# Kernel tuning notes

Measured on AMD Instinct MI355X. Metric: run time of the kernel, lower is better.

## Reference

```python
import jax, jax.numpy as jnp
import numpy as np

N = 50000   # nodes
E = 200000  # edges (avg degree ~4, pose-graph-like sparsity)
F_IN = 512
NEG_SLOPE = 0.01  # F.leaky_relu default


def _softmax_aggr(src_feat, dst, num_nodes):
    # torch_geometric SoftmaxAggregation(t=1): per-destination, per-feature
    # alpha = softmax(x_j), out = sum_j alpha * x_j
    m = jax.ops.segment_max(src_feat, dst, num_segments=num_nodes)  # [N,F]
    m = jnp.where(jnp.isfinite(m), m, 0.0)  # empty segments -> -inf guard
    e = jnp.exp(src_feat - m[dst])                                   # [E,F]
    denom = jax.ops.segment_sum(e, dst, num_segments=num_nodes)      # [N,F]
    num = jax.ops.segment_sum(e * src_feat, dst, num_segments=num_nodes)
    return num / jnp.maximum(denom, 1e-16)  # 0 for isolated nodes


def setup_inputs() -> dict:
    key = jax.random.key(0)
    ks = jax.random.split(key, 9)
    inp = {
        "x": jax.random.normal(ks[0], (N, F_IN), dtype=jnp.float32),
        "W1_rel": jax.random.normal(ks[1], (513, 256), dtype=jnp.float32) * 0.04,
        "b1_rel": jnp.zeros((256,), dtype=jnp.float32),
        "W1_root": jax.random.normal(ks[2], (513, 256), dtype=jnp.float32) * 0.04,
        "W2_rel": jax.random.normal(ks[3], (257, 64), dtype=jnp.float32) * 0.06,
        "b2_rel": jnp.zeros((64,), dtype=jnp.float32),
        "W2_root": jax.random.normal(ks[4], (257, 64), dtype=jnp.float32) * 0.06,
        "Wp": jax.random.normal(ks[5], (65, 3), dtype=jnp.float32) * 0.1,
        "bp": jnp.zeros((3,), dtype=jnp.float32),
        "Wr": jax.random.normal(ks[6], (65, 4), dtype=jnp.float32) * 0.1,
        "br": jnp.zeros((4,), dtype=jnp.float32),
        "edge_index": jax.random.randint(ks[7], (2, E), 0, N, dtype=jnp.int64),
    }
    return inp


def reference(x, W1_rel, b1_rel, W1_root, W2_rel, b2_rel, W2_root,
              Wp, bp, Wr, br, edge_index):
    src, dst = edge_index[0], edge_index[1]
    node_index = jnp.arange(x.shape[0], dtype=x.dtype)[:, None]  # [N,1]

    # dropout is identity in eval mode
    h = jnp.concatenate([x, node_index], axis=1)  # [N,513]

    # GraphConv(513,256, aggr='softmax'): lin_rel(softmax_aggr(x_j)) + lin_root(x)
    agg1 = _softmax_aggr(h[src], dst, x.shape[0])               # [N,513]
    h = agg1 @ W1_rel + b1_rel + h @ W1_root                     # [N,256]
    h = jnp.where(h >= 0, h, NEG_SLOPE * h)

    h = jnp.concatenate([h, node_index], axis=1)  # [N,257]

    # GraphConv(257,64) default aggr='add'
    agg2 = jax.ops.segment_sum(h[src], dst, num_segments=x.shape[0])  # [N,257]
    h = agg2 @ W2_rel + b2_rel + h @ W2_root                           # [N,64]
    h = jnp.where(h >= 0, h, NEG_SLOPE * h)

    h = jnp.concatenate([h, node_index], axis=1)  # [N,65]

    position = h @ Wp + bp                         # [N,3]
    rotation = h @ Wr + br                         # [N,4]
    norm = jnp.linalg.norm(rotation, axis=1, keepdims=True)
    rotation = rotation / jnp.maximum(norm, 1e-12)  # F.normalize

    return jnp.concatenate([position, rotation], axis=1)  # [N,7]
```

## Files before the change

kernel.cpp:

```cpp
#include <hip/hip_runtime.h>

#define NNODES 50000
#define NEDGES 200000
#define NSCANB ((NNODES + 255) / 256)

typedef short  bf16x8 __attribute__((ext_vector_type(8)));
typedef float  f32x4  __attribute__((ext_vector_type(4)));
typedef unsigned int u32x4 __attribute__((ext_vector_type(4)));

__device__ __forceinline__ unsigned short f2bf(float f) {
    union { float f; unsigned int u; } c; c.f = f;
    unsigned int r = c.u + 0x7fffu + ((c.u >> 16) & 1u);
    return (unsigned short)(r >> 16);
}
__device__ __forceinline__ float bflo(unsigned int v) {
    union { unsigned int u; float f; } c; c.u = v << 16;
    return c.f;
}
__device__ __forceinline__ float bfhi(unsigned int v) {
    union { unsigned int u; float f; } c; c.u = v & 0xffff0000u;
    return c.f;
}

#define PREP_B1 (256 * 1024)
#define PREP_B2 (64 * 512)
#define PREP_XC (NNODES * 64)
__global__ __launch_bounds__(256) void k_prepcount(const float* __restrict__ x,
                                                   const float* __restrict__ W1_rel,
                                                   const float* __restrict__ W1_root,
                                                   const float* __restrict__ W2_rel,
                                                   const float* __restrict__ W2_root,
                                                   const int* __restrict__ ei,
                                                   int* __restrict__ deg,
                                                   unsigned short* __restrict__ Bt1,
                                                   unsigned short* __restrict__ Bt2,
                                                   unsigned short* __restrict__ xb) {
    const int gtid = blockIdx.x * 256 + threadIdx.x;
    const int GS = gridDim.x * 256;
    for (int e = gtid; e < NEDGES; e += GS) atomicAdd(&deg[ei[NEDGES + e]], 1);
    for (int i = gtid; i < PREP_B1; i += GS) {
        int n = i >> 10, k = i & 1023;
        float v = (k < 512) ? W1_rel[k * 256 + n] : W1_root[(k - 512) * 256 + n];
        Bt1[i] = f2bf(v);
    }
    for (int i = gtid; i < PREP_B2; i += GS) {
        int n = i >> 9, k = i & 511;
        float v = (k < 256) ? W2_rel[k * 64 + n] : W2_root[(k - 256) * 64 + n];
        Bt2[i] = f2bf(v);
    }
    for (int i = gtid; i < PREP_XC; i += GS) {
        int n = i >> 6, c8 = (i & 63) * 8;
        const float* xp = x + (size_t)n * 512 + c8;
        float4 a = *(const float4*)xp;
        float4 bb = *(const float4*)(xp + 4);
        unsigned short o[8];
        o[0] = f2bf(a.x); o[1] = f2bf(a.y); o[2] = f2bf(a.z); o[3] = f2bf(a.w);
        o[4] = f2bf(bb.x); o[5] = f2bf(bb.y); o[6] = f2bf(bb.z); o[7] = f2bf(bb.w);
        *(u32x4*)(xb + (size_t)n * 512 + c8) = *(const u32x4*)o;
    }
}

__global__ __launch_bounds__(256) void k_scanA(const int* __restrict__ deg,
                                               int* __restrict__ rs,
                                               int* __restrict__ partials) {
    __shared__ int sm[256];
    int t = threadIdx.x, i = blockIdx.x * 256 + t;
    int v = (i < NNODES) ? deg[i] : 0;
    sm[t] = v;
    __syncthreads();
#pragma unroll
    for (int off = 1; off < 256; off <<= 1) {
        int u = (t >= off) ? sm[t - off] : 0;
        __syncthreads();
        sm[t] += u;
        __syncthreads();
    }
    if (i < NNODES) rs[i] = sm[t] - v;
    if (t == 255) partials[blockIdx.x] = sm[255];
}

__global__ __launch_bounds__(256) void k_scanC2(int* __restrict__ rs,
                                                const int* __restrict__ partials,
                                                int* __restrict__ cursor) {
    __shared__ int sm[256];
    int t = threadIdx.x, b = blockIdx.x;
    sm[t] = (t < b && t < NSCANB) ? partials[t] : 0;
    __syncthreads();
#pragma unroll
    for (int off = 128; off; off >>= 1) {
        if (t < off) sm[t] += sm[t + off];
        __syncthreads();
    }
    int off0 = sm[0];
    int i = b * 256 + t;
    if (i < NNODES) {
        int rv = rs[i] + off0;
        rs[i] = rv;
        cursor[i] = rv;
    }
    if (i == 0) rs[NNODES] = NEDGES;
}

__global__ void k_scatter(const int* __restrict__ ei, int* __restrict__ cursor,
                          int* __restrict__ srcs) {
    int e = blockIdx.x * 256 + threadIdx.x;
    if (e < NEDGES) {
        int d = ei[NEDGES + e];
        int p = atomicAdd(&cursor[d], 1);
        srcs[p] = ei[e];
    }
}

__global__ __launch_bounds__(256) void k_agg1(const unsigned short* __restrict__ xb,
                                              const int* __restrict__ rs,
                                              const int* __restrict__ srcs,
                                              unsigned short* __restrict__ AggBuf) {
    int wv = threadIdx.x >> 6;
    int lane = threadIdx.x & 63;
    int n = blockIdx.x * 4 + wv;
    int e0 = rs[n], e1 = rs[n + 1];
    float nu[8], de[8];
#pragma unroll
    for (int j = 0; j < 8; ++j) { nu[j] = 0.f; de[j] = 0.f; }

    auto accum = [&](u32x4 r) {
#pragma unroll
        for (int p = 0; p < 4; ++p) {
            float v0 = bflo(r[p]), v1 = bfhi(r[p]);
            float E0 = __expf(v0), E1 = __expf(v1);
            de[2 * p] += E0; nu[2 * p] += E0 * v0;
            de[2 * p + 1] += E1; nu[2 * p + 1] += E1 * v1;
        }
    };

    int e = e0;
    for (; e + 3 < e1; e += 4) {
        int s0 = srcs[e], s1 = srcs[e + 1], s2 = srcs[e + 2], s3 = srcs[e + 3];
        u32x4 r0 = *(const u32x4*)(xb + (size_t)s0 * 512 + lane * 8);
        u32x4 r1 = *(const u32x4*)(xb + (size_t)s1 * 512 + lane * 8);
        u32x4 r2 = *(const u32x4*)(xb + (size_t)s2 * 512 + lane * 8);
        u32x4 r3 = *(const u32x4*)(xb + (size_t)s3 * 512 + lane * 8);
        accum(r0); accum(r1); accum(r2); accum(r3);
    }
    if (e + 1 < e1) {
        int s0 = srcs[e], s1 = srcs[e + 1];
        u32x4 r0 = *(const u32x4*)(xb + (size_t)s0 * 512 + lane * 8);
        u32x4 r1 = *(const u32x4*)(xb + (size_t)s1 * 512 + lane * 8);
        accum(r0); accum(r1);
        e += 2;
    }
    if (e < e1) {
        u32x4 r0 = *(const u32x4*)(xb + (size_t)srcs[e] * 512 + lane * 8);
        accum(r0);
    }
    unsigned short o[8];
#pragma unroll
    for (int j = 0; j < 8; ++j) o[j] = f2bf(nu[j] / fmaxf(de[j], 1e-16f));
    *(u32x4*)(AggBuf + (size_t)n * 512 + lane * 8) = *(const u32x4*)o;
}

__global__ __launch_bounds__(256) void k_agg2(const int* __restrict__ rs,
                                              const int* __restrict__ srcs,
                                              const unsigned short* __restrict__ H1,
                                              unsigned short* __restrict__ Seg) {
    int wv = threadIdx.x >> 6;
    int lane = threadIdx.x & 63;
    int n = blockIdx.x * 4 + wv;
    int e0 = rs[n], e1 = rs[n + 1];
    float a[4] = {0.f, 0.f, 0.f, 0.f};

    auto accum = [&](uint2 r) {
        a[0] += bflo(r.x); a[1] += bfhi(r.x);
        a[2] += bflo(r.y); a[3] += bfhi(r.y);
    };

    int e = e0;
    for (; e + 3 < e1; e += 4) {
        int s0 = srcs[e], s1 = srcs[e + 1], s2 = srcs[e + 2], s3 = srcs[e + 3];
        uint2 r0 = *(const uint2*)(H1 + (size_t)s0 * 256 + lane * 4);
        uint2 r1 = *(const uint2*)(H1 + (size_t)s1 * 256 + lane * 4);
        uint2 r2 = *(const uint2*)(H1 + (size_t)s2 * 256 + lane * 4);
        uint2 r3 = *(const uint2*)(H1 + (size_t)s3 * 256 + lane * 4);
        accum(r0); accum(r1); accum(r2); accum(r3);
    }
    if (e + 1 < e1) {
        int s0 = srcs[e], s1 = srcs[e + 1];
        uint2 r0 = *(const uint2*)(H1 + (size_t)s0 * 256 + lane * 4);
        uint2 r1 = *(const uint2*)(H1 + (size_t)s1 * 256 + lane * 4);
        accum(r0); accum(r1);
        e += 2;
    }
    if (e < e1) {
        uint2 r0 = *(const uint2*)(H1 + (size_t)srcs[e] * 256 + lane * 4);
        accum(r0);
    }
    uint2 o;
    o.x = (unsigned int)f2bf(a[0]) | ((unsigned int)f2bf(a[1]) << 16);
    o.y = (unsigned int)f2bf(a[2]) | ((unsigned int)f2bf(a[3]) << 16);
    *(uint2*)(Seg + (size_t)n * 256 + lane * 4) = o;
}

__global__ __launch_bounds__(256) void k_gemm1(const unsigned short* __restrict__ A1,
                                               const unsigned short* __restrict__ A2,
                                               const unsigned short* __restrict__ Bt,
                                               const int* __restrict__ rs,
                                               const int* __restrict__ srcs,
                                               const float* __restrict__ r1,
                                               const float* __restrict__ r2,
                                               const float* __restrict__ bias,
                                               unsigned short* __restrict__ outp) {
    constexpr int BM = 64, BN = 128, BK = 64;
    __shared__ __align__(16) unsigned short As[2][BM * BK];
    __shared__ __align__(16) unsigned short Bs[2][BN * BK];
    __shared__ float s1t[BM];

    const int tid = threadIdx.x;
    const int w = tid >> 6;
    const int lane = tid & 63;
    const int lm = lane & 15;
    const int quad = lane >> 4;
    const int wr = w >> 1;
    const int wc = w & 1;
    const int rowbase = blockIdx.y * BM;
    const int colbase = blockIdx.x * BN;
    const int wrow = wr * 32;
    const int wcol = wc * 64;

    const int rsub = lane >> 3;
    const int csw = (lane & 7) ^ rsub;

    f32x4 acc[2][4];
#pragma unroll
    for (int mi = 0; mi < 2; ++mi)
#pragma unroll
        for (int ni = 0; ni < 4; ++ni) acc[mi][ni] = (f32x4){0.f, 0.f, 0.f, 0.f};

    auto stage = [&](unsigned short* Asb, unsigned short* Bsb, int kt) {
        const unsigned short* Ab = (kt < 512) ? A1 : A2;
        int kof = (kt < 512) ? kt : kt - 512;
#pragma unroll
        for (int l = 0; l < 2; ++l) {
            int r = w * 16 + l * 8;
            int gr = rowbase + r + rsub;
            if (gr >= NNODES) gr = NNODES - 1;
            const unsigned short* gp = Ab + (size_t)gr * 512 + kof + csw * 8;
            __builtin_amdgcn_global_load_lds(
                (const __attribute__((address_space(1))) void*)gp,
                (__attribute__((address_space(3))) void*)(Asb + r * BK), 16, 0, 0);
        }
#pragma unroll
        for (int l = 0; l < 4; ++l) {
            int r = w * 32 + l * 8;
            const unsigned short* gp = Bt + (size_t)(colbase + r + rsub) * 1024 + kt + csw * 8;
            __builtin_amdgcn_global_load_lds(
                (const __attribute__((address_space(1))) void*)gp,
                (__attribute__((address_space(3))) void*)(Bsb + r * BK), 16, 0, 0);
        }
    };

    auto compute = [&](const unsigned short* Asb, const unsigned short* Bsb) {
#pragma unroll
        for (int kk = 0; kk < BK; kk += 32) {
            const int kidx = (kk >> 3) + quad;
            const int phys = kidx ^ (lm & 7);
            bf16x8 af[2], bfr[4];
#pragma unroll
            for (int mi = 0; mi < 2; ++mi)
                af[mi] = __builtin_bit_cast(bf16x8,
                    *(const u32x4*)(Asb + (wrow + mi * 16 + lm) * BK + phys * 8));
#pragma unroll
            for (int ni = 0; ni < 4; ++ni)
                bfr[ni] = __builtin_bit_cast(bf16x8,
                    *(const u32x4*)(Bsb + (wcol + ni * 16 + lm) * BK + phys * 8));
#pragma unroll
            for (int mi = 0; mi < 2; ++mi)
#pragma unroll
                for (int ni = 0; ni < 4; ++ni)
                    acc[mi][ni] = __builtin_amdgcn_mfma_f32_16x16x32_bf16(
                        af[mi], bfr[ni], acc[mi][ni], 0, 0, 0);
        }
    };

    stage(As[0], Bs[0], 0);
#pragma unroll 1
    for (int t = 0; t < 16; t += 2) {
        stage(As[1], Bs[1], (t + 1) * BK);
        asm volatile("s_waitcnt vmcnt(6)" ::: "memory");
        __builtin_amdgcn_s_barrier();
        __builtin_amdgcn_sched_barrier(0);
        compute(As[0], Bs[0]);
        __builtin_amdgcn_s_barrier();
        if (t + 2 < 16) {
            stage(As[0], Bs[0], (t + 2) * BK);
            asm volatile("s_waitcnt vmcnt(6)" ::: "memory");
        } else {
            asm volatile("s_waitcnt vmcnt(0)" ::: "memory");
        }
        __builtin_amdgcn_s_barrier();
        __builtin_amdgcn_sched_barrier(0);
        compute(As[1], Bs[1]);
        __builtin_amdgcn_s_barrier();
    }

    if (tid < BM) {
        int grow = rowbase + tid;
        float r_ = 0.f;
        if (grow < NNODES) {
            int e0 = rs[grow], e1 = rs[grow + 1];
            float m = -INFINITY, d = 0.f, q = 0.f;
            for (int e = e0; e < e1; ++e) {
                float v = (float)srcs[e];
                float nm = fmaxf(m, v);
                float sc = __expf(m - nm), ee = __expf(v - nm);
                d = d * sc + ee;
                q = q * sc + ee * v;
                m = nm;
            }
            r_ = q / fmaxf(d, 1e-16f);
        }
        s1t[tid] = r_;
    }
    __syncthreads();

#pragma unroll
    for (int ni = 0; ni < 4; ++ni) {
        int gc = colbase + wcol + ni * 16 + lm;
        float r1v = r1[gc], r2v = r2[gc], bv = bias[gc];
#pragma unroll
        for (int mi = 0; mi < 2; ++mi) {
#pragma unroll
            for (int r = 0; r < 4; ++r) {
                int lrow = wrow + mi * 16 + quad * 4 + r;
                int grow = rowbase + lrow;
                if (grow < NNODES) {
                    float v = acc[mi][ni][r] + s1t[lrow] * r1v + (float)grow * r2v + bv;
                    v = (v >= 0.f) ? v : 0.01f * v;
                    outp[(size_t)grow * 256 + gc] = f2bf(v);
                }
            }
        }
    }
}

__global__ __launch_bounds__(256) void k_gemm2h(const unsigned short* __restrict__ A1,
                                                const unsigned short* __restrict__ A2,
                                                const unsigned short* __restrict__ Bt,
                                                const int* __restrict__ rs,
                                                const int* __restrict__ srcs,
                                                const float* __restrict__ r1,
                                                const float* __restrict__ r2,
                                                const float* __restrict__ bias,
                                                const float* __restrict__ Wp,
                                                const float* __restrict__ bp,
                                                const float* __restrict__ Wr,
                                                const float* __restrict__ br,
                                                float* __restrict__ out) {
    constexpr int BM = 64, BN = 64, BK = 64;
    __shared__ __align__(16) unsigned short As[BM * BK];
    __shared__ __align__(16) unsigned short Bs[BN * BK];
    __shared__ float h2t[BM * 65];
    __shared__ float s1t[BM];

    const int tid = threadIdx.x;
    const int w = tid >> 6;
    const int lane = tid & 63;
    const int lm = lane & 15;
    const int quad = lane >> 4;
    const int rowbase = blockIdx.x * BM;
    const int wrow = w * 16;

    const int rsub = lane >> 3;
    const int csw = (lane & 7) ^ rsub;

    f32x4 acc[4];
#pragma unroll
    for (int ni = 0; ni < 4; ++ni) acc[ni] = (f32x4){0.f, 0.f, 0.f, 0.f};

    for (int kt = 0; kt < 512; kt += BK) {
        const unsigned short* Ab = (kt < 256) ? A1 : A2;
        int kof = (kt < 256) ? kt : kt - 256;
#pragma unroll
        for (int l = 0; l < 2; ++l) {
            int r = w * 16 + l * 8;
            int gr = rowbase + r + rsub;
            if (gr >= NNODES) gr = NNODES - 1;
            const unsigned short* gp = Ab + (size_t)gr * 256 + kof + csw * 8;
            __builtin_amdgcn_global_load_lds(
                (const __attribute__((address_space(1))) void*)gp,
                (__attribute__((address_space(3))) void*)(As + r * BK), 16, 0, 0);
        }
#pragma unroll
        for (int l = 0; l < 2; ++l) {
            int r = w * 16 + l * 8;
            const unsigned short* gp = Bt + (size_t)(r + rsub) * 512 + kt + csw * 8;
            __builtin_amdgcn_global_load_lds(
                (const __attribute__((address_space(1))) void*)gp,
                (__attribute__((address_space(3))) void*)(Bs + r * BK), 16, 0, 0);
        }
        __syncthreads();
#pragma unroll
        for (int kk = 0; kk < BK; kk += 32) {
            const int kidx = (kk >> 3) + quad;
            const int phys = kidx ^ (lm & 7);
            bf16x8 af;
            af = __builtin_bit_cast(bf16x8,
                *(const u32x4*)(As + (wrow + lm) * BK + phys * 8));
            bf16x8 bfr[4];
#pragma unroll
            for (int ni = 0; ni < 4; ++ni)
                bfr[ni] = __builtin_bit_cast(bf16x8,
                    *(const u32x4*)(Bs + (ni * 16 + lm) * BK + phys * 8));
#pragma unroll
            for (int ni = 0; ni < 4; ++ni)
                acc[ni] = __builtin_amdgcn_mfma_f32_16x16x32_bf16(
                    af, bfr[ni], acc[ni], 0, 0, 0);
        }
        __syncthreads();
    }

    if (tid < BM) {
        int grow = rowbase + tid;
        float si = 0.f;
        if (grow < NNODES) {
            int e0 = rs[grow], e1 = rs[grow + 1];
            for (int e = e0; e < e1; ++e) si += (float)srcs[e];
        }
        s1t[tid] = si;
    }
    __syncthreads();

#pragma unroll
    for (int ni = 0; ni < 4; ++ni) {
        int gc = ni * 16 + lm;
        float r1v = r1[gc], r2v = r2[gc], bv = bias[gc];
#pragma unroll
        for (int r = 0; r < 4; ++r) {
            int lrow = wrow + quad * 4 + r;
            int grow = rowbase + lrow;
            float v = acc[ni][r] + s1t[lrow] * r1v + (float)grow * r2v + bv;
            v = (v >= 0.f) ? v : 0.01f * v;
            h2t[lrow * 65 + gc] = v;
        }
    }
    __syncthreads();

    if (tid < BM) {
        int grow = rowbase + tid;
        if (grow < NNODES) {
            const float* hv = h2t + tid * 65;
            float idx = (float)grow;
            float p0 = 0.f, p1 = 0.f, p2 = 0.f;
            float r0 = 0.f, r1a = 0.f, r2a = 0.f, r3 = 0.f;
#pragma unroll 8
            for (int c = 0; c < 64; ++c) {
                float v = hv[c];
                p0 += v * Wp[c * 3 + 0];
                p1 += v * Wp[c * 3 + 1];
                p2 += v * Wp[c * 3 + 2];
                r0 += v * Wr[c * 4 + 0];
                r1a += v * Wr[c * 4 + 1];
                r2a += v * Wr[c * 4 + 2];
                r3 += v * Wr[c * 4 + 3];
            }
            p0 += idx * Wp[64 * 3 + 0] + bp[0];
            p1 += idx * Wp[64 * 3 + 1] + bp[1];
            p2 += idx * Wp[64 * 3 + 2] + bp[2];
            r0 += idx * Wr[64 * 4 + 0] + br[0];
            r1a += idx * Wr[64 * 4 + 1] + br[1];
            r2a += idx * Wr[64 * 4 + 2] + br[2];
            r3 += idx * Wr[64 * 4 + 3] + br[3];
            float nrm = fmaxf(sqrtf(r0 * r0 + r1a * r1a + r2a * r2a + r3 * r3), 1e-12f);
            float* op = out + (size_t)grow * 7;
            op[0] = p0; op[1] = p1; op[2] = p2;
            op[3] = r0 / nrm; op[4] = r1a / nrm; op[5] = r2a / nrm; op[6] = r3 / nrm;
        }
    }
}

extern "C" void kernel_launch(void* const* d_in, const int* in_sizes, int n_in,
                              void* d_out, int out_size, void* d_ws, size_t ws_size,
                              hipStream_t stream) {
    const float* x       = (const float*)d_in[0];
    const float* W1_rel  = (const float*)d_in[1];
    const float* b1      = (const float*)d_in[2];
    const float* W1_root = (const float*)d_in[3];
    const float* W2_rel  = (const float*)d_in[4];
    const float* b2      = (const float*)d_in[5];
    const float* W2_root = (const float*)d_in[6];
    const float* Wp      = (const float*)d_in[7];
    const float* bp      = (const float*)d_in[8];
    const float* Wr      = (const float*)d_in[9];
    const float* br      = (const float*)d_in[10];
    const int*   ei      = (const int*)d_in[11];
    float* out = (float*)d_out;

    char* ws = (char*)d_ws;
    size_t off = 0;
    auto alloc = [&](size_t bytes) {
        size_t o = off;
        off = (off + bytes + 255) & ~(size_t)255;
        return (void*)(ws + o);
    };
    int*   deg       = (int*)alloc(NNODES * 4);
    int*   cursor    = (int*)alloc(NNODES * 4);
    int*   row_start = (int*)alloc((NNODES + 1) * 4);
    int*   srcs      = (int*)alloc(NEDGES * 4);
    int*   partials  = (int*)alloc(NSCANB * 4);
    unsigned short* xb     = (unsigned short*)alloc((size_t)NNODES * 512 * 2);
    unsigned short* AggBuf = (unsigned short*)alloc((size_t)NNODES * 512 * 2);
    unsigned short* H1     = (unsigned short*)alloc((size_t)NNODES * 256 * 2);
    unsigned short* Seg    = (unsigned short*)alloc((size_t)NNODES * 256 * 2);
    unsigned short* Bt1    = (unsigned short*)alloc(256 * 1024 * 2);
    unsigned short* Bt2    = (unsigned short*)alloc(64 * 512 * 2);

    hipMemsetAsync(deg, 0, NNODES * 4, stream);

    k_prepcount<<<2048, 256, 0, stream>>>(
        x, W1_rel, W1_root, W2_rel, W2_root, ei, deg, Bt1, Bt2, xb);

    k_scanA<<<NSCANB, 256, 0, stream>>>(deg, row_start, partials);
    k_scanC2<<<NSCANB, 256, 0, stream>>>(row_start, partials, cursor);
    k_scatter<<<(NEDGES + 255) / 256, 256, 0, stream>>>(ei, cursor, srcs);

    k_agg1<<<NNODES / 4, 256, 0, stream>>>(xb, row_start, srcs, AggBuf);

    k_gemm1<<<dim3(2, (NNODES + 63) / 64), 256, 0, stream>>>(
        AggBuf, xb, Bt1, row_start, srcs, W1_rel + 512 * 256, W1_root + 512 * 256, b1, H1);

    k_agg2<<<NNODES / 4, 256, 0, stream>>>(row_start, srcs, H1, Seg);

    k_gemm2h<<<(NNODES + 63) / 64, 256, 0, stream>>>(
        Seg, H1, Bt2, row_start, srcs, W2_rel + 256 * 64, W2_root + 256 * 64, b2,
        Wp, bp, Wr, br, out);
}
```

Measured before the change: 339.7 us.

## Load GEMM weight fragments directly from global into registers, drop B LDS staging

Both GEMM kernels stop staging the B (weight) tile through LDS and have each lane load its MFMA B fragments straight from global memory into registers, relying on the cache because the weights are small and shared by every block. In k_gemm1 this also removes the double-buffered A/B pipeline and replaces it with a single-buffer loop that synchronises twice per K step. The aim is to cut LDS traffic and LDS footprint, which may allow more resident blocks. In exchange, global B loads now sit on the critical path with no prefetch, and the overlap of loads with compute in gemm1 is lost.

```diff
diff --git a/kernel.cpp b/kernel.cpp
--- a/kernel.cpp
+++ b/kernel.cpp
@@ -210,8 +210,7 @@
                                                const float* __restrict__ bias,
                                                unsigned short* __restrict__ outp) {
     constexpr int BM = 64, BN = 128, BK = 64;
-    __shared__ __align__(16) unsigned short As[2][BM * BK];
-    __shared__ __align__(16) unsigned short Bs[2][BN * BK];
+    __shared__ __align__(16) unsigned short As[BM * BK];
     __shared__ float s1t[BM];
 
     const int tid = threadIdx.x;
@@ -229,13 +228,16 @@
     const int rsub = lane >> 3;
     const int csw = (lane & 7) ^ rsub;
 
+    const unsigned short* bbase = Bt + (size_t)(colbase + wcol + lm) * 1024 + quad * 8;
+
     f32x4 acc[2][4];
 #pragma unroll
     for (int mi = 0; mi < 2; ++mi)
 #pragma unroll
         for (int ni = 0; ni < 4; ++ni) acc[mi][ni] = (f32x4){0.f, 0.f, 0.f, 0.f};
 
-    auto stage = [&](unsigned short* Asb, unsigned short* Bsb, int kt) {
+#pragma unroll 1
+    for (int kt = 0; kt < 1024; kt += BK) {
         const unsigned short* Ab = (kt < 512) ? A1 : A2;
         int kof = (kt < 512) ? kt : kt - 512;
 #pragma unroll
@@ -246,60 +248,34 @@
             const unsigned short* gp = Ab + (size_t)gr * 512 + kof + csw * 8;
             __builtin_amdgcn_global_load_lds(
                 (const __attribute__((address_space(1))) void*)gp,
-                (__attribute__((address_space(3))) void*)(Asb + r * BK), 16, 0, 0);
-        }
-#pragma unroll
-        for (int l = 0; l < 4; ++l) {
-            int r = w * 32 + l * 8;
-            const unsigned short* gp = Bt + (size_t)(colbase + r + rsub) * 1024 + kt + csw * 8;
-            __builtin_amdgcn_global_load_lds(
-                (const __attribute__((address_space(1))) void*)gp,
-                (__attribute__((address_space(3))) void*)(Bsb + r * BK), 16, 0, 0);
-        }
-    };
-
-    auto compute = [&](const unsigned short* Asb, const unsigned short* Bsb) {
-#pragma unroll
-        for (int kk = 0; kk < BK; kk += 32) {
-            const int kidx = (kk >> 3) + quad;
+                (__attribute__((address_space(3))) void*)(As + r * BK), 16, 0, 0);
+        }
+        bf16x8 breg[2][4];
+#pragma unroll
+        for (int h = 0; h < 2; ++h) {
+#pragma unroll
+            for (int ni = 0; ni < 4; ++ni)
+                breg[h][ni] = __builtin_bit_cast(bf16x8,
+                    *(const u32x4*)(bbase + (size_t)ni * 16 * 1024 + kt + h * 32));
+        }
+        __syncthreads();
+#pragma unroll
+        for (int h = 0; h < 2; ++h) {
+            const int kidx = h * 4 + quad;
             const int phys = kidx ^ (lm & 7);
-            bf16x8 af[2], bfr[4];
+            bf16x8 af[2];
 #pragma unroll
             for (int mi = 0; mi < 2; ++mi)
                 af[mi] = __builtin_bit_cast(bf16x8,
-                    *(const u32x4*)(Asb + (wrow + mi * 16 + lm) * BK + phys * 8));
-#pragma unroll
-            for (int ni = 0; ni < 4; ++ni)
-                bfr[ni] = __builtin_bit_cast(bf16x8,
-                    *(const u32x4*)(Bsb + (wcol + ni * 16 + lm) * BK + phys * 8));
+                    *(const u32x4*)(As + (wrow + mi * 16 + lm) * BK + phys * 8));
 #pragma unroll
             for (int mi = 0; mi < 2; ++mi)
 #pragma unroll
                 for (int ni = 0; ni < 4; ++ni)
                     acc[mi][ni] = __builtin_amdgcn_mfma_f32_16x16x32_bf16(
-                        af[mi], bfr[ni], acc[mi][ni], 0, 0, 0);
-        }
-    };
-
-    stage(As[0], Bs[0], 0);
-#pragma unroll 1
-    for (int t = 0; t < 16; t += 2) {
-        stage(As[1], Bs[1], (t + 1) * BK);
-        asm volatile("s_waitcnt vmcnt(6)" ::: "memory");
-        __builtin_amdgcn_s_barrier();
-        __builtin_amdgcn_sched_barrier(0);
-        compute(As[0], Bs[0]);
-        __builtin_amdgcn_s_barrier();
-        if (t + 2 < 16) {
-            stage(As[0], Bs[0], (t + 2) * BK);
-            asm volatile("s_waitcnt vmcnt(6)" ::: "memory");
-        } else {
-            asm volatile("s_waitcnt vmcnt(0)" ::: "memory");
-        }
-        __builtin_amdgcn_s_barrier();
-        __builtin_amdgcn_sched_barrier(0);
-        compute(As[1], Bs[1]);
-        __builtin_amdgcn_s_barrier();
+                        af[mi], breg[h][ni], acc[mi][ni], 0, 0, 0);
+        }
+        __syncthreads();
     }
 
     if (tid < BM) {
@@ -357,7 +333,6 @@
                                                 float* __restrict__ out) {
     constexpr int BM = 64, BN = 64, BK = 64;
     __shared__ __align__(16) unsigned short As[BM * BK];
-    __shared__ __align__(16) unsigned short Bs[BN * BK];
     __shared__ float h2t[BM * 65];
     __shared__ float s1t[BM];
 
@@ -372,10 +347,13 @@
     const int rsub = lane >> 3;
     const int csw = (lane & 7) ^ rsub;
 
+    const unsigned short* bbase = Bt + (size_t)lm * 512 + quad * 8;
+
     f32x4 acc[4];
 #pragma unroll
     for (int ni = 0; ni < 4; ++ni) acc[ni] = (f32x4){0.f, 0.f, 0.f, 0.f};
 
+#pragma unroll 1
     for (int kt = 0; kt < 512; kt += BK) {
         const unsigned short* Ab = (kt < 256) ? A1 : A2;
         int kof = (kt < 256) ? kt : kt - 256;
@@ -389,31 +367,25 @@
                 (const __attribute__((address_space(1))) void*)gp,
                 (__attribute__((address_space(3))) void*)(As + r * BK), 16, 0, 0);
         }
-#pragma unroll
-        for (int l = 0; l < 2; ++l) {
-            int r = w * 16 + l * 8;
-            const unsigned short* gp = Bt + (size_t)(r + rsub) * 512 + kt + csw * 8;
-            __builtin_amdgcn_global_load_lds(
-                (const __attribute__((address_space(1))) void*)gp,
-                (__attribute__((address_space(3))) void*)(Bs + r * BK), 16, 0, 0);
-        }
-        __syncthreads();
-#pragma unroll
-        for (int kk = 0; kk < BK; kk += 32) {
-            const int kidx = (kk >> 3) + quad;
+        bf16x8 breg[2][4];
+#pragma unroll
+        for (int h = 0; h < 2; ++h) {
+#pragma unroll
+            for (int ni = 0; ni < 4; ++ni)
+                breg[h][ni] = __builtin_bit_cast(bf16x8,
+                    *(const u32x4*)(bbase + (size_t)ni * 16 * 512 + kt + h * 32));
+        }
+        __syncthreads();
+#pragma unroll
+        for (int h = 0; h < 2; ++h) {
+            const int kidx = h * 4 + quad;
             const int phys = kidx ^ (lm & 7);
-            bf16x8 af;
-            af = __builtin_bit_cast(bf16x8,
+            bf16x8 af = __builtin_bit_cast(bf16x8,
                 *(const u32x4*)(As + (wrow + lm) * BK + phys * 8));
-            bf16x8 bfr[4];
-#pragma unroll
-            for (int ni = 0; ni < 4; ++ni)
-                bfr[ni] = __builtin_bit_cast(bf16x8,
-                    *(const u32x4*)(Bs + (ni * 16 + lm) * BK + phys * 8));
 #pragma unroll
             for (int ni = 0; ni < 4; ++ni)
                 acc[ni] = __builtin_amdgcn_mfma_f32_16x16x32_bf16(
-                    af, bfr[ni], acc[ni], 0, 0, 0);
+                    af, breg[h][ni], acc[ni], 0, 0, 0);
         }
         __syncthreads();
     }
```

Result: slower. 417.8 us (+23.0%).

## Enlarge GEMM1 row tile to 128 and use single-buffered LDS staging

Applied to the files above, without the earlier changes.

Doubles the row tile of the first GEMM so each block computes 128x128 outputs with a 4x4 MFMA accumulator grid per wave, halving the number of row blocks and the B-tile reloads. The hand-written double-buffered pipeline with explicit vmcnt waits is replaced by a simple load, sync, compute, sync loop on a single LDS buffer. This improves operand reuse and reduces grid size but removes load/compute overlap and raises register pressure.

```diff
diff --git a/kernel.cpp b/kernel.cpp
--- a/kernel.cpp
+++ b/kernel.cpp
@@ -209,9 +209,9 @@
                                                const float* __restrict__ r2,
                                                const float* __restrict__ bias,
                                                unsigned short* __restrict__ outp) {
-    constexpr int BM = 64, BN = 128, BK = 64;
-    __shared__ __align__(16) unsigned short As[2][BM * BK];
-    __shared__ __align__(16) unsigned short Bs[2][BN * BK];
+    constexpr int BM = 128, BN = 128, BK = 64;
+    __shared__ __align__(16) unsigned short As[BM * BK];
+    __shared__ __align__(16) unsigned short Bs[BN * BK];
     __shared__ float s1t[BM];
 
     const int tid = threadIdx.x;
@@ -223,30 +223,31 @@
     const int wc = w & 1;
     const int rowbase = blockIdx.y * BM;
     const int colbase = blockIdx.x * BN;
-    const int wrow = wr * 32;
+    const int wrow = wr * 64;
     const int wcol = wc * 64;
 
     const int rsub = lane >> 3;
     const int csw = (lane & 7) ^ rsub;
 
-    f32x4 acc[2][4];
-#pragma unroll
-    for (int mi = 0; mi < 2; ++mi)
+    f32x4 acc[4][4];
+#pragma unroll
+    for (int mi = 0; mi < 4; ++mi)
 #pragma unroll
         for (int ni = 0; ni < 4; ++ni) acc[mi][ni] = (f32x4){0.f, 0.f, 0.f, 0.f};
 
-    auto stage = [&](unsigned short* Asb, unsigned short* Bsb, int kt) {
+#pragma unroll 1
+    for (int kt = 0; kt < 1024; kt += BK) {
         const unsigned short* Ab = (kt < 512) ? A1 : A2;
         int kof = (kt < 512) ? kt : kt - 512;
 #pragma unroll
-        for (int l = 0; l < 2; ++l) {
-            int r = w * 16 + l * 8;
+        for (int l = 0; l < 4; ++l) {
+            int r = w * 32 + l * 8;
             int gr = rowbase + r + rsub;
             if (gr >= NNODES) gr = NNODES - 1;
             const unsigned short* gp = Ab + (size_t)gr * 512 + kof + csw * 8;
             __builtin_amdgcn_global_load_lds(
                 (const __attribute__((address_space(1))) void*)gp,
-                (__attribute__((address_space(3))) void*)(Asb + r * BK), 16, 0, 0);
+                (__attribute__((address_space(3))) void*)(As + r * BK), 16, 0, 0);
         }
 #pragma unroll
         for (int l = 0; l < 4; ++l) {
@@ -254,52 +255,30 @@
             const unsigned short* gp = Bt + (size_t)(colbase + r + rsub) * 1024 + kt + csw * 8;
             __builtin_amdgcn_global_load_lds(
                 (const __attribute__((address_space(1))) void*)gp,
-                (__attribute__((address_space(3))) void*)(Bsb + r * BK), 16, 0, 0);
-        }
-    };
-
-    auto compute = [&](const unsigned short* Asb, const unsigned short* Bsb) {
+                (__attribute__((address_space(3))) void*)(Bs + r * BK), 16, 0, 0);
+        }
+        __syncthreads();
 #pragma unroll
         for (int kk = 0; kk < BK; kk += 32) {
             const int kidx = (kk >> 3) + quad;
             const int phys = kidx ^ (lm & 7);
-            bf16x8 af[2], bfr[4];
-#pragma unroll
-            for (int mi = 0; mi < 2; ++mi)
+            bf16x8 af[4], bfr[4];
+#pragma unroll
+            for (int mi = 0; mi < 4; ++mi)
                 af[mi] = __builtin_bit_cast(bf16x8,
-                    *(const u32x4*)(Asb + (wrow + mi * 16 + lm) * BK + phys * 8));
+                    *(const u32x4*)(As + (wrow + mi * 16 + lm) * BK + phys * 8));
 #pragma unroll
             for (int ni = 0; ni < 4; ++ni)
                 bfr[ni] = __builtin_bit_cast(bf16x8,
-                    *(const u32x4*)(Bsb + (wcol + ni * 16 + lm) * BK + phys * 8));
-#pragma unroll
-            for (int mi = 0; mi < 2; ++mi)
+                    *(const u32x4*)(Bs + (wcol + ni * 16 + lm) * BK + phys * 8));
+#pragma unroll
+            for (int mi = 0; mi < 4; ++mi)
 #pragma unroll
                 for (int ni = 0; ni < 4; ++ni)
                     acc[mi][ni] = __builtin_amdgcn_mfma_f32_16x16x32_bf16(
                         af[mi], bfr[ni], acc[mi][ni], 0, 0, 0);
         }
-    };
-
-    stage(As[0], Bs[0], 0);
-#pragma unroll 1
-    for (int t = 0; t < 16; t += 2) {
-        stage(As[1], Bs[1], (t + 1) * BK);
-        asm volatile("s_waitcnt vmcnt(6)" ::: "memory");
-        __builtin_amdgcn_s_barrier();
-        __builtin_amdgcn_sched_barrier(0);
-        compute(As[0], Bs[0]);
-        __builtin_amdgcn_s_barrier();
-        if (t + 2 < 16) {
-            stage(As[0], Bs[0], (t + 2) * BK);
-            asm volatile("s_waitcnt vmcnt(6)" ::: "memory");
-        } else {
-            asm volatile("s_waitcnt vmcnt(0)" ::: "memory");
-        }
-        __builtin_amdgcn_s_barrier();
-        __builtin_amdgcn_sched_barrier(0);
-        compute(As[1], Bs[1]);
-        __builtin_amdgcn_s_barrier();
+        __syncthreads();
     }
 
     if (tid < BM) {
@@ -327,7 +306,7 @@
         int gc = colbase + wcol + ni * 16 + lm;
         float r1v = r1[gc], r2v = r2[gc], bv = bias[gc];
 #pragma unroll
-        for (int mi = 0; mi < 2; ++mi) {
+        for (int mi = 0; mi < 4; ++mi) {
 #pragma unroll
             for (int r = 0; r < 4; ++r) {
                 int lrow = wrow + mi * 16 + quad * 4 + r;
@@ -524,7 +503,7 @@
 
     k_agg1<<<NNODES / 4, 256, 0, stream>>>(xb, row_start, srcs, AggBuf);
 
-    k_gemm1<<<dim3(2, (NNODES + 63) / 64), 256, 0, stream>>>(
+    k_gemm1<<<dim3(2, (NNODES + 127) / 128), 256, 0, stream>>>(
         AggBuf, xb, Bt1, row_start, srcs, W1_rel + 512 * 256, W1_root + 512 * 256, b1, H1);
 
     k_agg2<<<NNODES / 4, 256, 0, stream>>>(row_start, srcs, H1, Seg);
```

Result: no change. 340.3 us (+0.2%).

## Fuse CSR build into cooperative kernel and enlarge gemm1 row tile

Applied to the files above, without the earlier changes.

Replaces the memset, degree count, two scan kernels and the scatter with a single cooperative kernel that uses grid-wide syncs between phases, cutting several launches and the gaps between them. Weight and x conversion moves to a separate prep kernel. Separately, gemm1 now uses a 128-row tile with 4x4 MFMA accumulators per wave, which raises register and LDS use per block and gives fewer blocks, in exchange for more reuse of each B tile.

```diff
diff --git a/kernel.cpp b/kernel.cpp
--- a/kernel.cpp
+++ b/kernel.cpp
@@ -1,4 +1,7 @@
 #include <hip/hip_runtime.h>
+#include <hip/hip_cooperative_groups.h>
+
+namespace cg = cooperative_groups;
 
 #define NNODES 50000
 #define NEDGES 200000
@@ -22,22 +25,69 @@
     return c.f;
 }
 
+__global__ __launch_bounds__(256) void k_graph(const int* __restrict__ ei,
+                                               int* __restrict__ deg,
+                                               int* __restrict__ rs,
+                                               int* __restrict__ cursor,
+                                               int* __restrict__ partials,
+                                               int* __restrict__ srcs) {
+    cg::grid_group grid = cg::this_grid();
+    __shared__ int sm[256];
+    const int t = threadIdx.x, b = blockIdx.x;
+    const int gtid = b * 256 + t;
+    const int GS = gridDim.x * 256;
+
+    for (int i = gtid; i < NNODES; i += GS) deg[i] = 0;
+    grid.sync();
+    for (int e = gtid; e < NEDGES; e += GS) atomicAdd(&deg[ei[NEDGES + e]], 1);
+    grid.sync();
+    const int i = gtid;
+    int v = (i < NNODES) ? deg[i] : 0;
+    sm[t] = v;
+    __syncthreads();
+#pragma unroll
+    for (int off = 1; off < 256; off <<= 1) {
+        int u = (t >= off) ? sm[t - off] : 0;
+        __syncthreads();
+        sm[t] += u;
+        __syncthreads();
+    }
+    const int local = sm[t] - v;
+    if (t == 255) partials[b] = sm[255];
+    grid.sync();
+    sm[t] = (t < b && t < NSCANB) ? partials[t] : 0;
+    __syncthreads();
+#pragma unroll
+    for (int off = 128; off; off >>= 1) {
+        if (t < off) sm[t] += sm[t + off];
+        __syncthreads();
+    }
+    {
+        int off0 = sm[0];
+        if (i < NNODES) { int rv = local + off0; rs[i] = rv; cursor[i] = rv; }
+        if (i == 0) rs[NNODES] = NEDGES;
+    }
+    grid.sync();
+    for (int e = gtid; e < NEDGES; e += GS) {
+        int d = ei[NEDGES + e];
+        int p = atomicAdd(&cursor[d], 1);
+        srcs[p] = ei[e];
+    }
+}
+
 #define PREP_B1 (256 * 1024)
 #define PREP_B2 (64 * 512)
 #define PREP_XC (NNODES * 64)
-__global__ __launch_bounds__(256) void k_prepcount(const float* __restrict__ x,
-                                                   const float* __restrict__ W1_rel,
-                                                   const float* __restrict__ W1_root,
-                                                   const float* __restrict__ W2_rel,
-                                                   const float* __restrict__ W2_root,
-                                                   const int* __restrict__ ei,
-                                                   int* __restrict__ deg,
-                                                   unsigned short* __restrict__ Bt1,
-                                                   unsigned short* __restrict__ Bt2,
-                                                   unsigned short* __restrict__ xb) {
+__global__ __launch_bounds__(256) void k_prep(const float* __restrict__ x,
+                                              const float* __restrict__ W1_rel,
+                                              const float* __restrict__ W1_root,
+                                              const float* __restrict__ W2_rel,
+                                              const float* __restrict__ W2_root,
+                                              unsigned short* __restrict__ Bt1,
+                                              unsigned short* __restrict__ Bt2,
+                                              unsigned short* __restrict__ xb) {
     const int gtid = blockIdx.x * 256 + threadIdx.x;
     const int GS = gridDim.x * 256;
-    for (int e = gtid; e < NEDGES; e += GS) atomicAdd(&deg[ei[NEDGES + e]], 1);
     for (int i = gtid; i < PREP_B1; i += GS) {
         int n = i >> 10, k = i & 1023;
         float v = (k < 512) ? W1_rel[k * 256 + n] : W1_root[(k - 512) * 256 + n];
@@ -60,57 +110,6 @@
     }
 }
 
-__global__ __launch_bounds__(256) void k_scanA(const int* __restrict__ deg,
-                                               int* __restrict__ rs,
-                                               int* __restrict__ partials) {
-    __shared__ int sm[256];
-    int t = threadIdx.x, i = blockIdx.x * 256 + t;
-    int v = (i < NNODES) ? deg[i] : 0;
-    sm[t] = v;
-    __syncthreads();
-#pragma unroll
-    for (int off = 1; off < 256; off <<= 1) {
-        int u = (t >= off) ? sm[t - off] : 0;
-        __syncthreads();
-        sm[t] += u;
-        __syncthreads();
-    }
-    if (i < NNODES) rs[i] = sm[t] - v;
-    if (t == 255) partials[blockIdx.x] = sm[255];
-}
-
-__global__ __launch_bounds__(256) void k_scanC2(int* __restrict__ rs,
-                                                const int* __restrict__ partials,
-                                                int* __restrict__ cursor) {
-    __shared__ int sm[256];
-    int t = threadIdx.x, b = blockIdx.x;
-    sm[t] = (t < b && t < NSCANB) ? partials[t] : 0;
-    __syncthreads();
-#pragma unroll
-    for (int off = 128; off; off >>= 1) {
-        if (t < off) sm[t] += sm[t + off];
-        __syncthreads();
-    }
-    int off0 = sm[0];
-    int i = b * 256 + t;
-    if (i < NNODES) {
-        int rv = rs[i] + off0;
-        rs[i] = rv;
-        cursor[i] = rv;
-    }
-    if (i == 0) rs[NNODES] = NEDGES;
-}
-
-__global__ void k_scatter(const int* __restrict__ ei, int* __restrict__ cursor,
-                          int* __restrict__ srcs) {
-    int e = blockIdx.x * 256 + threadIdx.x;
-    if (e < NEDGES) {
-        int d = ei[NEDGES + e];
-        int p = atomicAdd(&cursor[d], 1);
-        srcs[p] = ei[e];
-    }
-}
-
 __global__ __launch_bounds__(256) void k_agg1(const unsigned short* __restrict__ xb,
                                               const int* __restrict__ rs,
                                               const int* __restrict__ srcs,
@@ -209,7 +208,7 @@
                                                const float* __restrict__ r2,
                                                const float* __restrict__ bias,
                                                unsigned short* __restrict__ outp) {
-    constexpr int BM = 64, BN = 128, BK = 64;
+    constexpr int BM = 128, BN = 128, BK = 64;
     __shared__ __align__(16) unsigned short As[2][BM * BK];
     __shared__ __align__(16) unsigned short Bs[2][BN * BK];
     __shared__ float s1t[BM];
@@ -223,15 +222,15 @@
     const int wc = w & 1;
     const int rowbase = blockIdx.y * BM;
     const int colbase = blockIdx.x * BN;
-    const int wrow = wr * 32;
+    const int wrow = wr * 64;
     const int wcol = wc * 64;
 
     const int rsub = lane >> 3;
     const int csw = (lane & 7) ^ rsub;
 
-    f32x4 acc[2][4];
-#pragma unroll
-    for (int mi = 0; mi < 2; ++mi)
+    f32x4 acc[4][4];
+#pragma unroll
+    for (int mi = 0; mi < 4; ++mi)
 #pragma unroll
         for (int ni = 0; ni < 4; ++ni) acc[mi][ni] = (f32x4){0.f, 0.f, 0.f, 0.f};
 
@@ -239,8 +238,8 @@
         const unsigned short* Ab = (kt < 512) ? A1 : A2;
         int kof = (kt < 512) ? kt : kt - 512;
 #pragma unroll
-        for (int l = 0; l < 2; ++l) {
-            int r = w * 16 + l * 8;
+        for (int l = 0; l < 4; ++l) {
+            int r = w * 32 + l * 8;
             int gr = rowbase + r + rsub;
             if (gr >= NNODES) gr = NNODES - 1;
             const unsigned short* gp = Ab + (size_t)gr * 512 + kof + csw * 8;
@@ -263,9 +262,9 @@
         for (int kk = 0; kk < BK; kk += 32) {
             const int kidx = (kk >> 3) + quad;
             const int phys = kidx ^ (lm & 7);
-            bf16x8 af[2], bfr[4];
-#pragma unroll
-            for (int mi = 0; mi < 2; ++mi)
+            bf16x8 af[4], bfr[4];
+#pragma unroll
+            for (int mi = 0; mi < 4; ++mi)
                 af[mi] = __builtin_bit_cast(bf16x8,
                     *(const u32x4*)(Asb + (wrow + mi * 16 + lm) * BK + phys * 8));
 #pragma unroll
@@ -273,7 +272,7 @@
                 bfr[ni] = __builtin_bit_cast(bf16x8,
                     *(const u32x4*)(Bsb + (wcol + ni * 16 + lm) * BK + phys * 8));
 #pragma unroll
-            for (int mi = 0; mi < 2; ++mi)
+            for (int mi = 0; mi < 4; ++mi)
 #pragma unroll
                 for (int ni = 0; ni < 4; ++ni)
                     acc[mi][ni] = __builtin_amdgcn_mfma_f32_16x16x32_bf16(
@@ -285,14 +284,14 @@
 #pragma unroll 1
     for (int t = 0; t < 16; t += 2) {
         stage(As[1], Bs[1], (t + 1) * BK);
-        asm volatile("s_waitcnt vmcnt(6)" ::: "memory");
+        asm volatile("s_waitcnt vmcnt(8)" ::: "memory");
         __builtin_amdgcn_s_barrier();
         __builtin_amdgcn_sched_barrier(0);
         compute(As[0], Bs[0]);
         __builtin_amdgcn_s_barrier();
         if (t + 2 < 16) {
             stage(As[0], Bs[0], (t + 2) * BK);
-            asm volatile("s_waitcnt vmcnt(6)" ::: "memory");
+            asm volatile("s_waitcnt vmcnt(8)" ::: "memory");
         } else {
             asm volatile("s_waitcnt vmcnt(0)" ::: "memory");
         }
@@ -327,7 +326,7 @@
         int gc = colbase + wcol + ni * 16 + lm;
         float r1v = r1[gc], r2v = r2[gc], bv = bias[gc];
 #pragma unroll
-        for (int mi = 0; mi < 2; ++mi) {
+        for (int mi = 0; mi < 4; ++mi) {
 #pragma unroll
             for (int r = 0; r < 4; ++r) {
                 int lrow = wrow + mi * 16 + quad * 4 + r;
@@ -513,18 +512,19 @@
     unsigned short* Bt1    = (unsigned short*)alloc(256 * 1024 * 2);
     unsigned short* Bt2    = (unsigned short*)alloc(64 * 512 * 2);
 
-    hipMemsetAsync(deg, 0, NNODES * 4, stream);
-
-    k_prepcount<<<2048, 256, 0, stream>>>(
-        x, W1_rel, W1_root, W2_rel, W2_root, ei, deg, Bt1, Bt2, xb);
-
-    k_scanA<<<NSCANB, 256, 0, stream>>>(deg, row_start, partials);
-    k_scanC2<<<NSCANB, 256, 0, stream>>>(row_start, partials, cursor);
-    k_scatter<<<(NEDGES + 255) / 256, 256, 0, stream>>>(ei, cursor, srcs);
+    {
+        void* kargs[] = {(void*)&ei, (void*)&deg, (void*)&row_start,
+                         (void*)&cursor, (void*)&partials, (void*)&srcs};
+        hipLaunchCooperativeKernel((void*)k_graph, dim3(NSCANB), dim3(256),
+                                   kargs, 0, stream);
+    }
+
+    k_prep<<<2048, 256, 0, stream>>>(
+        x, W1_rel, W1_root, W2_rel, W2_root, Bt1, Bt2, xb);
 
     k_agg1<<<NNODES / 4, 256, 0, stream>>>(xb, row_start, srcs, AggBuf);
 
-    k_gemm1<<<dim3(2, (NNODES + 63) / 64), 256, 0, stream>>>(
+    k_gemm1<<<dim3(2, (NNODES + 127) / 128), 256, 0, stream>>>(
         AggBuf, xb, Bt1, row_start, srcs, W1_rel + 512 * 256, W1_root + 512 * 256, b1, H1);
 
     k_agg2<<<NNODES / 4, 256, 0, stream>>>(row_start, srcs, H1, Seg);
```

Measured after the change: 444.9 us. 1.31x slower.
